# Optimization experiments

Hardware: AMD Instinct MI355X
Metric: run time of the kernel (lower is better)

Reference implementation:

```python
import jax, jax.numpy as jnp
import numpy as np

H_DIM = 1152
N_HEADS = 12
HEAD_DIM = H_DIM // N_HEADS  # 96, divisible by 3
SCALE_ROT = 32 // 16  # character_pixel_size // patch_size


def setup_inputs() -> dict:
    key = jax.random.key(0)
    ks = jax.random.split(key, 9)
    std = 1.0 / np.sqrt(H_DIM)
    return {
        "hidden_states": jax.random.normal(ks[0], (8, 1025, H_DIM), dtype=jnp.float32),
        "Wq": jax.random.normal(ks[1], (H_DIM, H_DIM), dtype=jnp.float32) * std,
        "bq": jax.random.normal(ks[2], (H_DIM,), dtype=jnp.float32) * 0.02,
        "Wk": jax.random.normal(ks[3], (H_DIM, H_DIM), dtype=jnp.float32) * std,
        "bk": jax.random.normal(ks[4], (H_DIM,), dtype=jnp.float32) * 0.02,
        "Wv": jax.random.normal(ks[5], (H_DIM, H_DIM), dtype=jnp.float32) * std,
        "bv": jax.random.normal(ks[6], (H_DIM,), dtype=jnp.float32) * 0.02,
        "Wo": jax.random.normal(ks[7], (H_DIM, H_DIM), dtype=jnp.float32) * std,
        "bo": jax.random.normal(ks[8], (H_DIM,), dtype=jnp.float32) * 0.02,
        "rows": 32,
        "cols": 32,
    }


def _rotary_tables(seq_len, rows, cols, dtype):
    # (seq_len, n_triplets) trig tables based on 2-D patch grid position
    inv_freq = 1.0 / (10000.0 ** (jnp.arange(0, HEAD_DIM, 3, dtype=dtype) / (HEAD_DIM * SCALE_ROT)))
    ids = jnp.arange(seq_len)
    cls_offset = 1 if seq_len != rows * cols else 0
    grid_ids = jnp.clip(ids - cls_offset, 0)
    row_ids = (grid_ids // cols).astype(dtype)
    col_ids = (grid_ids % cols).astype(dtype)
    theta = row_ids[:, None] * inv_freq
    psi = col_ids[:, None] * inv_freq
    return jnp.cos(theta), jnp.sin(theta), jnp.cos(psi), jnp.sin(psi)


def _apply_rotary_3d(x, ct, st, cp, sp):
    # x: (b, s, h, d) -> view as (b, s, h, t, 3)
    b, s, h, d = x.shape
    x = x.reshape(b, s, h, d // 3, 3)
    ct = ct[None, :, None, :]
    st = st[None, :, None, :]
    cp = cp[None, :, None, :]
    sp = sp[None, :, None, :]
    x0, x1, x2 = x[..., 0], x[..., 1], x[..., 2]
    r0 = cp * x0 + sp * st * x1 + sp * ct * x2
    r1 = ct * x1 - st * x2
    r2 = -sp * x0 + cp * st * x1 + cp * ct * x2
    return jnp.stack((r0, r1, r2), axis=-1).reshape(b, s, h, d)


def reference(hidden_states, Wq, bq, Wk, bk, Wv, bv, Wo, bo, rows, cols):
    b, s, _ = hidden_states.shape
    dtype = hidden_states.dtype
    scale = HEAD_DIM ** -0.5

    q = (hidden_states @ Wq + bq).reshape(b, s, N_HEADS, HEAD_DIM)
    k = (hidden_states @ Wk + bk).reshape(b, s, N_HEADS, HEAD_DIM)
    v = (hidden_states @ Wv + bv).reshape(b, s, N_HEADS, HEAD_DIM)

    ct, st, cp, sp = _rotary_tables(s, rows, cols, dtype)
    q = _apply_rotary_3d(q, ct, st, cp, sp)
    k = _apply_rotary_3d(k, ct, st, cp, sp)

    # (b, h, s, s) attention scores
    scores = jnp.einsum("bqhd,bkhd->bhqk", q, k) * scale
    probs = jax.nn.softmax(scores.astype(jnp.float32), axis=-1).astype(dtype)
    ctx = jnp.einsum("bhqk,bkhd->bqhd", probs, v).reshape(b, s, H_DIM)
    out = ctx @ Wo + bo
    return out
```

## Files before the change

### kernel.cpp

```cpp
#include <hip/hip_runtime.h>
#include <stdint.h>

#define BATCH 8
#define SEQ   1025
#define HDIM  1152
#define NH    12
#define DH    96
#define MROWS (BATCH*SEQ)
#define N_QKV (3*HDIM)
#define KD    HDIM
#define NT2   18

typedef __attribute__((ext_vector_type(8))) short short8;
typedef __attribute__((ext_vector_type(4))) short short4_;
typedef __attribute__((ext_vector_type(4))) float float4_;
typedef __attribute__((ext_vector_type(16))) float f32x16;

#define AS1 __attribute__((address_space(1)))
#define AS3 __attribute__((address_space(3)))
#define BARM() do { asm volatile("" ::: "memory"); __builtin_amdgcn_s_barrier(); asm volatile("" ::: "memory"); } while (0)
#define LGKM0() do { asm volatile("s_waitcnt lgkmcnt(0)" ::: "memory"); __builtin_amdgcn_sched_barrier(0); } while (0)

__device__ inline float bf2f(short s) {
  union { unsigned u; float f; } x; x.u = ((unsigned)(unsigned short)s) << 16; return x.f;
}
__device__ inline short f2bf(float f) {
  union { float f; unsigned u; } x; x.f = f;
  unsigned r = (x.u + 0x7fffu + ((x.u >> 16) & 1u)) >> 16;
  return (short)r;
}

__global__ __launch_bounds__(256) void convx(const float* __restrict__ hs, short* __restrict__ X) {
  int i = blockIdx.x * 256 + threadIdx.x;
  float4_ v = ((const float4_*)hs)[i];
  short4_ o;
  o[0] = f2bf(v[0]); o[1] = f2bf(v[1]); o[2] = f2bf(v[2]); o[3] = f2bf(v[3]);
  ((short4_*)X)[i] = o;
}

__global__ __launch_bounds__(256) void convw_t(const float* __restrict__ W0,
                                               const float* __restrict__ W1,
                                               const float* __restrict__ W2,
                                               short* __restrict__ Wt) {
  __shared__ float T[64][65];
  const int z = blockIdx.z;
  const float* W = z == 0 ? W0 : (z == 1 ? W1 : W2);
  const int n0 = blockIdx.x * 64, k0 = blockIdx.y * 64;
  const int tid = threadIdx.x;
  const int r = tid >> 2, cq = (tid & 3) * 16;
#pragma unroll
  for (int u = 0; u < 4; ++u) {
    float4_ v = *(const float4_*)&W[(long)(k0 + r) * HDIM + n0 + cq + u * 4];
    T[r][cq + u * 4 + 0] = v[0]; T[r][cq + u * 4 + 1] = v[1];
    T[r][cq + u * 4 + 2] = v[2]; T[r][cq + u * 4 + 3] = v[3];
  }
  __syncthreads();
  const int n = tid >> 2, kq = (tid & 3) * 16;
  short out[16];
#pragma unroll
  for (int u = 0; u < 16; ++u) out[u] = f2bf(T[kq + u][n]);
  short* dst = Wt + (long)(z * HDIM + n0 + n) * KD + k0 + kq;
  *(short8*)dst = *(short8*)&out[0];
  *(short8*)(dst + 8) = *(short8*)&out[8];
}

template<int OUTF32>
__global__ __launch_bounds__(512, 2) void gemm256(
    const short* __restrict__ A, const short* __restrict__ Bt,
    const float* __restrict__ b0, const float* __restrict__ b1, const float* __restrict__ b2,
    void* __restrict__ Cout, const int N, const int MT) {
  __shared__ alignas(16) short Lds[65536];
  const int tid = threadIdx.x;
  const int l = tid & 63, w = tid >> 6;
  const int lrow = l & 15, lg = l >> 4;
  const int wr = w >> 2, wc = w & 3;

  const int nwg = gridDim.x;
  const int qq = nwg >> 3, r8 = nwg & 7;
  const int xcd = blockIdx.x & 7, loc = blockIdx.x >> 3;
  const int wg = (xcd < r8 ? xcd * (qq + 1) : r8 * (qq + 1) + (xcd - r8) * qq) + loc;
  const int mt = wg % MT, nt = wg / MT;
  const int m0 = mt * 256, n0 = nt * 256;

  const short* asrc[2]; const short* bsrc[2];
#pragma unroll
  for (int i = 0; i < 2; ++i) {
    int p = i * 512 + tid;
    int wl = (p & 7) ^ ((p >> 3) & 7);
    int row = ((p >> 3) << 1) | (wl >> 2);
    int kc = (wl & 3) * 8;
    int ra = m0 + row; if (ra > MROWS - 1) ra = MROWS - 1;
    int rb = n0 + row; if (rb > N - 1) rb = N - 1;
    asrc[i] = A + (long)ra * KD + kc;
    bsrc[i] = Bt + (long)rb * KD + kc;
  }

#define STAGEA(sb, kh, kt_, i) \
  __builtin_amdgcn_global_load_lds((const AS1 void*)(asrc[i] + (kt_) * 64 + (kh) * 32), \
      (AS3 void*)(&Lds[(sb) * 16384 + (kh) * 8192 + (i * 512 + tid) * 8]), 16, 0, 0)
#define STAGEB(sb, kh, kt_, i) \
  __builtin_amdgcn_global_load_lds((const AS1 void*)(bsrc[i] + (kt_) * 64 + (kh) * 32), \
      (AS3 void*)(&Lds[32768 + (sb) * 16384 + (kh) * 8192 + (i * 512 + tid) * 8]), 16, 0, 0)
#define LDA(dst, base, mi) { const int row_ = wr * 128 + (mi) * 16 + lrow; \
  dst = *(const short8*)&Lds[(base) + ((row_ >> 1) << 6) + \
      (((((row_ & 1) << 2) + lg) ^ ((row_ >> 1) & 7)) << 3)]; }
#define LDB(dst, base, nj) { const int row_ = wc * 64 + (nj) * 16 + lrow; \
  dst = *(const short8*)&Lds[(base) + ((row_ >> 1) << 6) + \
      (((((row_ & 1) << 2) + lg) ^ ((row_ >> 1) & 7)) << 3)]; }
#define MFMA16(a, b, c) __builtin_amdgcn_mfma_f32_16x16x32_bf16(a, b, c, 0, 0, 0)
#define MF16(mb, A0, A1, A2, A3) \
  acc[(mb)+0][0] = MFMA16(A0, bf0, acc[(mb)+0][0]); \
  acc[(mb)+0][1] = MFMA16(A0, bf1, acc[(mb)+0][1]); \
  acc[(mb)+0][2] = MFMA16(A0, bf2, acc[(mb)+0][2]); \
  acc[(mb)+0][3] = MFMA16(A0, bf3, acc[(mb)+0][3]); \
  acc[(mb)+1][0] = MFMA16(A1, bf0, acc[(mb)+1][0]); \
  acc[(mb)+1][1] = MFMA16(A1, bf1, acc[(mb)+1][1]); \
  acc[(mb)+1][2] = MFMA16(A1, bf2, acc[(mb)+1][2]); \
  acc[(mb)+1][3] = MFMA16(A1, bf3, acc[(mb)+1][3]); \
  acc[(mb)+2][0] = MFMA16(A2, bf0, acc[(mb)+2][0]); \
  acc[(mb)+2][1] = MFMA16(A2, bf1, acc[(mb)+2][1]); \
  acc[(mb)+2][2] = MFMA16(A2, bf2, acc[(mb)+2][2]); \
  acc[(mb)+2][3] = MFMA16(A2, bf3, acc[(mb)+2][3]); \
  acc[(mb)+3][0] = MFMA16(A3, bf0, acc[(mb)+3][0]); \
  acc[(mb)+3][1] = MFMA16(A3, bf1, acc[(mb)+3][1]); \
  acc[(mb)+3][2] = MFMA16(A3, bf2, acc[(mb)+3][2]); \
  acc[(mb)+3][3] = MFMA16(A3, bf3, acc[(mb)+3][3]);

  float4_ acc[8][4];
#pragma unroll
  for (int mi = 0; mi < 8; ++mi)
#pragma unroll
    for (int nj = 0; nj < 4; ++nj) acc[mi][nj] = (float4_)(0.f);

  STAGEA(0, 0, 0, 0); STAGEA(0, 0, 0, 1);
  STAGEB(0, 0, 0, 0); STAGEB(0, 0, 0, 1);
  STAGEA(0, 1, 0, 0); STAGEA(0, 1, 0, 1);
  STAGEB(0, 1, 0, 0); STAGEB(0, 1, 0, 1);
  asm volatile("s_waitcnt vmcnt(4)" ::: "memory");
  BARM();

  for (int kt = 0; kt < NT2; ++kt) {
    const int cb = kt & 1, sb = (kt + 1) & 1;
    const bool dost = (kt + 1) < NT2;
    const int aK0 = cb * 16384, aK1 = aK0 + 8192;
    const int bK0 = 32768 + cb * 16384, bK1 = bK0 + 8192;
    short8 af0, af1, af2, af3, bf0, bf1, bf2, bf3;

    LDB(bf0, bK0, 0); LDB(bf1, bK0, 1); LDB(bf2, bK0, 2); LDB(bf3, bK0, 3);
    LDA(af0, aK0, 0); LDA(af1, aK0, 1); LDA(af2, aK0, 2); LDA(af3, aK0, 3);
    if (dost) { STAGEA(sb, 0, kt + 1, 0); STAGEA(sb, 0, kt + 1, 1); }
    BARM();
    LGKM0();
    __builtin_amdgcn_s_setprio(1);
    MF16(0, af0, af1, af2, af3);
    __builtin_amdgcn_s_setprio(0);
    BARM();
    LDA(af0, aK0, 4); LDA(af1, aK0, 5); LDA(af2, aK0, 6); LDA(af3, aK0, 7);
    if (dost) { STAGEB(sb, 0, kt + 1, 0); STAGEB(sb, 0, kt + 1, 1); }
    BARM();
    LGKM0();
    __builtin_amdgcn_s_setprio(1);
    MF16(4, af0, af1, af2, af3);
    __builtin_amdgcn_s_setprio(0);
    if (dost) asm volatile("s_waitcnt vmcnt(4)" ::: "memory");
    else      asm volatile("s_waitcnt vmcnt(0)" ::: "memory");
    BARM();
    LDB(bf0, bK1, 0); LDB(bf1, bK1, 1); LDB(bf2, bK1, 2); LDB(bf3, bK1, 3);
    LDA(af0, aK1, 0); LDA(af1, aK1, 1); LDA(af2, aK1, 2); LDA(af3, aK1, 3);
    if (dost) { STAGEA(sb, 1, kt + 1, 0); STAGEA(sb, 1, kt + 1, 1); }
    BARM();
    LGKM0();
    __builtin_amdgcn_s_setprio(1);
    MF16(0, af0, af1, af2, af3);
    __builtin_amdgcn_s_setprio(0);
    BARM();
    LDA(af0, aK1, 4); LDA(af1, aK1, 5); LDA(af2, aK1, 6); LDA(af3, aK1, 7);
    if (dost) { STAGEB(sb, 1, kt + 1, 0); STAGEB(sb, 1, kt + 1, 1); }
    BARM();
    LGKM0();
    __builtin_amdgcn_s_setprio(1);
    MF16(4, af0, af1, af2, af3);
    __builtin_amdgcn_s_setprio(0);
    if (dost) asm volatile("s_waitcnt vmcnt(4)" ::: "memory");
    BARM();
  }

  float bias[4];
#pragma unroll
  for (int nj = 0; nj < 4; ++nj) {
    int cn = n0 + wc * 64 + nj * 16 + lrow;
    float bv_ = 0.f;
    if (cn < N) bv_ = (N == HDIM) ? b0[cn]
                                  : (cn < HDIM ? b0[cn] : (cn < 2 * HDIM ? b1[cn - HDIM] : b2[cn - 2 * HDIM]));
    bias[nj] = bv_;
  }
#pragma unroll
  for (int mi = 0; mi < 8; ++mi)
#pragma unroll
    for (int r = 0; r < 4; ++r) {
      int m = m0 + wr * 128 + mi * 16 + lg * 4 + r;
      if (m >= MROWS) continue;
#pragma unroll
      for (int nj = 0; nj < 4; ++nj) {
        int cn = n0 + wc * 64 + nj * 16 + lrow;
        if (cn >= N) continue;
        float v = acc[mi][nj][r] + bias[nj];
        if (OUTF32) ((float*)Cout)[(long)m * N + cn] = v;
        else        ((short*)Cout)[(long)m * N + cn] = f2bf(v);
      }
    }
#undef STAGEA
#undef STAGEB
#undef LDA
#undef LDB
#undef MFMA16
#undef MF16
}

__global__ __launch_bounds__(256) void rotary_q(short* __restrict__ QKV,
                                                const int* __restrict__ rowsp,
                                                const int* __restrict__ colsp) {
  int idx = blockIdx.x * 256 + threadIdx.x;
  if (idx >= MROWS * NH * 4) return;
  const int qt = idx & 3;
  const int hm = idx >> 2;
  const int h = hm % NH, m = hm / NH;
  const int s = m % SEQ;
  const int cols = colsp[0], rws = rowsp[0];
  const int off = (SEQ != rws * cols) ? 1 : 0;
  int gid = s - off; if (gid < 0) gid = 0;
  const float frow = (float)(gid / cols), fcol = (float)(gid % cols);
  union { short sh[24]; short8 v[3]; } u;
  short* p = QKV + (long)m * N_QKV + h * DH + qt * 24;
  u.v[0] = *(short8*)p; u.v[1] = *(short8*)(p + 8); u.v[2] = *(short8*)(p + 16);
#pragma unroll
  for (int t = 0; t < 8; ++t) {
    int j = qt * 8 + t;
    float invf = exp2f((float)(3 * j) * (-13.287712379549449f / 192.0f));
    float st, ct, sp, cp;
    __sincosf(frow * invf, &st, &ct);
    __sincosf(fcol * invf, &sp, &cp);
    float x0 = bf2f(u.sh[3 * t]), x1 = bf2f(u.sh[3 * t + 1]), x2 = bf2f(u.sh[3 * t + 2]);
    u.sh[3 * t]     = f2bf( cp * x0 + sp * st * x1 + sp * ct * x2);
    u.sh[3 * t + 1] = f2bf( ct * x1 - st * x2);
    u.sh[3 * t + 2] = f2bf(-sp * x0 + cp * st * x1 + cp * ct * x2);
  }
  *(short8*)p = u.v[0]; *(short8*)(p + 8) = u.v[1]; *(short8*)(p + 16) = u.v[2];
}

__global__ __launch_bounds__(256) void fragpack(const short* __restrict__ QKV,
                                                short* __restrict__ Kf,
                                                short* __restrict__ Vf,
                                                const int* __restrict__ rowsp,
                                                const int* __restrict__ colsp) {
  __shared__ short L[64 * 96];
  const int t = blockIdx.x, bh = blockIdx.y;
  const int b = bh / NH, h = bh % NH;
  const int tid = threadIdx.x;
#pragma unroll
  for (int i = 0; i < 3; ++i) {
    int cc = i * 256 + tid;
    int kv = cc / 384;
    int rm = cc % 384;
    int r = rm / 12, m = rm % 12;
    int s = t * 32 + r; if (s > SEQ - 1) s = SEQ - 1;
    const short* src = QKV + (long)(b * SEQ + s) * N_QKV + (kv ? 2 * HDIM : HDIM) + h * DH + m * 8;
    *(short8*)&L[cc * 8] = *(const short8*)src;
  }
  __syncthreads();
  {
    const int cols = colsp[0], rws = rowsp[0];
    const int off = (SEQ != rws * cols) ? 1 : 0;
#pragma unroll
    for (int i = 0; i < 4; ++i) {
      int idx2 = i * 256 + tid;
      int r = idx2 >> 5, j = idx2 & 31;
      int s = t * 32 + r; if (s > SEQ - 1) s = SEQ - 1;
      int gid = s - off; if (gid < 0) gid = 0;
      float invf = exp2f((float)(3 * j) * (-13.287712379549449f / 192.0f));
      float st, ct, sp, cp;
      __sincosf((float)(gid / cols) * invf, &st, &ct);
      __sincosf((float)(gid % cols) * invf, &sp, &cp);
      short* pp = &L[r * 96 + 3 * j];
      float x0 = bf2f(pp[0]), x1 = bf2f(pp[1]), x2 = bf2f(pp[2]);
      pp[0] = f2bf( cp * x0 + sp * st * x1 + sp * ct * x2);
      pp[1] = f2bf( ct * x1 - st * x2);
      pp[2] = f2bf(-sp * x0 + cp * st * x1 + cp * ct * x2);
    }
  }
  __syncthreads();
#pragma unroll
  for (int i = 0; i < 3; ++i) {
    int oc = i * 256 + tid;
    if (oc < 384) {
      int c = oc / 64, ll = oc & 63;
      int qi = ll & 31, hi = ll >> 5;
      short8 v = *(const short8*)&L[qi * 96 + c * 16 + hi * 8];
      *(short8*)(Kf + (((long)(bh * 33 + t) * 6 + c) * 64 + ll) * 8) = v;
    } else {
      int oc2 = oc - 384;
      int d = oc2 / 128, sl = (oc2 / 64) & 1, ll = oc2 & 63;
      int qi = ll & 31, hi = ll >> 5;
      short8 v;
#pragma unroll
      for (int j = 0; j < 8; ++j)
        v[j] = L[32 * 96 + (sl * 16 + hi * 8 + j) * 96 + d * 32 + qi];
      *(short8*)(Vf + ((((long)(bh * 33 + t) * 3 + d) * 2 + sl) * 64 + ll) * 8) = v;
    }
  }
}

__global__ __launch_bounds__(128, 3) void attn_kernel(const short* __restrict__ QKV,
                                                      const short* __restrict__ Kf,
                                                      const short* __restrict__ Vf,
                                                      short* __restrict__ CTX) {
  const int tid = threadIdx.x;
  const int l = tid & 63, w = tid >> 6;
  const int qi = l & 31, hi = l >> 5;
  const int bid = blockIdx.x;
  const int xcd = bid & 7, jj = bid >> 3;
  const int bh = xcd * 12 + jj / 17;
  const int qb = jj % 17;
  const int b = bh / NH, h = bh % NH;
  const int s = qb * 64 + w * 32 + qi;
  const int sq = s > SEQ - 1 ? SEQ - 1 : s;

  const float scale = 0.1020620726159658f;
  const short* Qr = QKV + (long)(b * SEQ + sq) * N_QKV + h * DH;
  short8 qf[6];
#pragma unroll
  for (int c = 0; c < 6; ++c) {
    short8 v = *(const short8*)(Qr + c * 16 + hi * 8);
#pragma unroll
    for (int j = 0; j < 8; ++j) v[j] = f2bf(bf2f(v[j]) * scale);
    qf[c] = v;
  }

  const short* Kb = Kf + (long)bh * 33 * 6 * 64 * 8;
  const short* Vb = Vf + (long)bh * 33 * 6 * 64 * 8;

  f32x16 ctxv[3];
#pragma unroll
  for (int d = 0; d < 3; ++d) ctxv[d] = (f32x16)(0.f);
  float m_ = -1e30f, l_ = 0.f;

  for (int t = 0; t < 33; ++t) {
    f32x16 S = (f32x16)(0.f);
#pragma unroll
    for (int c = 0; c < 6; ++c) {
      short8 kf = *(const short8*)(Kb + (((long)t * 6 + c) * 64 + l) * 8);
      S = __builtin_amdgcn_mfma_f32_32x32x16_bf16(kf, qf[c], S, 0, 0, 0);
    }
    if (t == 32) {
      S[0] = hi ? -1e30f : S[0];
#pragma unroll
      for (int r = 1; r < 16; ++r) S[r] = -1e30f;
    }
    float tm = S[0];
#pragma unroll
    for (int r = 1; r < 16; ++r) tm = fmaxf(tm, S[r]);
    tm = fmaxf(tm, __shfl_xor(tm, 32));
    if (!__all(tm - m_ <= 8.f)) {
      float mn = fmaxf(m_, tm);
      float alpha = __expf(m_ - mn);
      m_ = mn;
      l_ *= alpha;
#pragma unroll
      for (int d = 0; d < 3; ++d)
#pragma unroll
        for (int r = 0; r < 16; ++r) ctxv[d][r] *= alpha;
    }
    float ts = 0.f;
#pragma unroll
    for (int r = 0; r < 16; ++r) { float p = __expf(S[r] - m_); S[r] = p; ts += p; }
    ts += __shfl_xor(ts, 32);
    l_ += ts;

    unsigned pk_[8];
#pragma unroll
    for (int j = 0; j < 8; ++j)
      pk_[j] = (unsigned)(unsigned short)f2bf(S[2 * j]) |
               ((unsigned)(unsigned short)f2bf(S[2 * j + 1]) << 16);
    unsigned s0 = hi ? pk_[0] : pk_[2];
    unsigned s1 = hi ? pk_[1] : pk_[3];
    unsigned s2 = hi ? pk_[4] : pk_[6];
    unsigned s3 = hi ? pk_[5] : pk_[7];
    unsigned r0 = __shfl_xor(s0, 32);
    unsigned r1 = __shfl_xor(s1, 32);
    unsigned r2 = __shfl_xor(s2, 32);
    unsigned r3 = __shfl_xor(s3, 32);
    union PF { unsigned u[4]; short8 s8; } f0, f1;
    f0.u[0] = hi ? r0 : pk_[0];
    f0.u[1] = hi ? r1 : pk_[1];
    f0.u[2] = hi ? pk_[2] : r0;
    f0.u[3] = hi ? pk_[3] : r1;
    f1.u[0] = hi ? r2 : pk_[4];
    f1.u[1] = hi ? r3 : pk_[5];
    f1.u[2] = hi ? pk_[6] : r2;
    f1.u[3] = hi ? pk_[7] : r3;

#pragma unroll
    for (int d = 0; d < 3; ++d) {
      const short* Vr = Vb + (((long)t * 3 + d) * 2 * 64) * 8;
      short8 vf0 = *(const short8*)(Vr + l * 8);
      ctxv[d] = __builtin_amdgcn_mfma_f32_32x32x16_bf16(vf0, f0.s8, ctxv[d], 0, 0, 0);
      short8 vf1 = *(const short8*)(Vr + (64 + l) * 8);
      ctxv[d] = __builtin_amdgcn_mfma_f32_32x32x16_bf16(vf1, f1.s8, ctxv[d], 0, 0, 0);
    }
  }

  float invl = 1.f / l_;
  if (s <= SEQ - 1) {
    short* Cr = CTX + (long)(b * SEQ + s) * HDIM + h * DH;
#pragma unroll
    for (int d = 0; d < 3; ++d)
#pragma unroll
      for (int g = 0; g < 4; ++g) {
        short4_ o;
#pragma unroll
        for (int r = 0; r < 4; ++r) o[r] = f2bf(ctxv[d][4 * g + r] * invl);
        *(short4_*)(Cr + d * 32 + 8 * g + 4 * hi) = o;
      }
  }
}

extern "C" void kernel_launch(void* const* d_in, const int* in_sizes, int n_in,
                              void* d_out, int out_size, void* d_ws, size_t ws_size,
                              hipStream_t stream) {
  const float* hs = (const float*)d_in[0];
  const float* Wq = (const float*)d_in[1];
  const float* bq = (const float*)d_in[2];
  const float* Wk = (const float*)d_in[3];
  const float* bk = (const float*)d_in[4];
  const float* Wv = (const float*)d_in[5];
  const float* bv = (const float*)d_in[6];
  const float* Wo = (const float*)d_in[7];
  const float* bo = (const float*)d_in[8];
  const int* rows = (const int*)d_in[9];
  const int* cols = (const int*)d_in[10];
  float* out = (float*)d_out;

  char* ws = (char*)d_ws;
  short* X   = (short*)(ws);
  short* Wt  = (short*)(ws + 18892800);
  short* Wot = (short*)(ws + 26855424);
  short* QKV = (short*)(ws + 29509632);
  short* Vf  = (short*)(ws + 86188032);
  short* CTX = (short*)(ws + 105652224);
  short* Kf  = (short*)(ws);

  convx<<<9225, 256, 0, stream>>>(hs, X);
  convw_t<<<dim3(18, 18, 3), 256, 0, stream>>>(Wq, Wk, Wv, Wt);
  convw_t<<<dim3(18, 18, 1), 256, 0, stream>>>(Wo, Wo, Wo, Wot);
  gemm256<0><<<462, 512, 0, stream>>>(X, Wt, bq, bk, bv, QKV, N_QKV, 33);
  rotary_q<<<1538, 256, 0, stream>>>(QKV, rows, cols);
  fragpack<<<dim3(33, 96), 256, 0, stream>>>(QKV, Kf, Vf, rows, cols);
  attn_kernel<<<1632, 128, 0, stream>>>(QKV, Kf, Vf, CTX);
  gemm256<1><<<165, 512, 0, stream>>>(CTX, Wot, bo, bo, bo, out, HDIM, 33);
}
```

Before: 275.3 us.

## Ping-pong wave groups in GEMM so LDS reads overlap MFMA of other half

Splits the 8 waves of the 256x256 GEMM into two groups by row half that alternate phases: one group reads its full A/B fragments from LDS while the other runs 32 MFMAs. Global-to-LDS staging for the next k-tile is issued as whole k-halves per phase, with adjusted vmcnt waits. The aim is to keep the matrix units busy while LDS reads are in flight. In exchange each thread holds 8 A fragments at once, raising register pressure under launch_bounds(512,2). It also relies on subtle barrier and waitcnt ordering for the shared double buffer.

After: 320.0 us. +16.2%, slower.

```diff
diff --git a/kernel.cpp b/kernel.cpp
--- a/kernel.cpp
+++ b/kernel.cpp
@@ -74,6 +74,7 @@
   const int l = tid & 63, w = tid >> 6;
   const int lrow = l & 15, lg = l >> 4;
   const int wr = w >> 2, wc = w & 3;
+  const bool isA = (wr == 0);
 
   const int nwg = gridDim.x;
   const int qq = nwg >> 3, r8 = nwg & 7;
@@ -101,12 +102,19 @@
 #define STAGEB(sb, kh, kt_, i) \
   __builtin_amdgcn_global_load_lds((const AS1 void*)(bsrc[i] + (kt_) * 64 + (kh) * 32), \
       (AS3 void*)(&Lds[32768 + (sb) * 16384 + (kh) * 8192 + (i * 512 + tid) * 8]), 16, 0, 0)
+#define STAGE_KH(sb, kh, kt_) do { \
+  STAGEA(sb, kh, kt_, 0); STAGEA(sb, kh, kt_, 1); \
+  STAGEB(sb, kh, kt_, 0); STAGEB(sb, kh, kt_, 1); } while (0)
 #define LDA(dst, base, mi) { const int row_ = wr * 128 + (mi) * 16 + lrow; \
   dst = *(const short8*)&Lds[(base) + ((row_ >> 1) << 6) + \
       (((((row_ & 1) << 2) + lg) ^ ((row_ >> 1) & 7)) << 3)]; }
 #define LDB(dst, base, nj) { const int row_ = wc * 64 + (nj) * 16 + lrow; \
   dst = *(const short8*)&Lds[(base) + ((row_ >> 1) << 6) + \
       (((((row_ & 1) << 2) + lg) ^ ((row_ >> 1) & 7)) << 3)]; }
+#define RD(aB, bB) do { \
+  LDB(bf0, bB, 0); LDB(bf1, bB, 1); LDB(bf2, bB, 2); LDB(bf3, bB, 3); \
+  LDA(af0, aB, 0); LDA(af1, aB, 1); LDA(af2, aB, 2); LDA(af3, aB, 3); \
+  LDA(af4, aB, 4); LDA(af5, aB, 5); LDA(af6, aB, 6); LDA(af7, aB, 7); } while (0)
 #define MFMA16(a, b, c) __builtin_amdgcn_mfma_f32_16x16x32_bf16(a, b, c, 0, 0, 0)
 #define MF16(mb, A0, A1, A2, A3) \
   acc[(mb)+0][0] = MFMA16(A0, bf0, acc[(mb)+0][0]); \
@@ -125,65 +133,49 @@
   acc[(mb)+3][1] = MFMA16(A3, bf1, acc[(mb)+3][1]); \
   acc[(mb)+3][2] = MFMA16(A3, bf2, acc[(mb)+3][2]); \
   acc[(mb)+3][3] = MFMA16(A3, bf3, acc[(mb)+3][3]);
+#define MF32() do { \
+  __builtin_amdgcn_s_setprio(1); \
+  MF16(0, af0, af1, af2, af3); \
+  MF16(4, af4, af5, af6, af7); \
+  __builtin_amdgcn_s_setprio(0); } while (0)
 
   float4_ acc[8][4];
 #pragma unroll
   for (int mi = 0; mi < 8; ++mi)
 #pragma unroll
     for (int nj = 0; nj < 4; ++nj) acc[mi][nj] = (float4_)(0.f);
-
-  STAGEA(0, 0, 0, 0); STAGEA(0, 0, 0, 1);
-  STAGEB(0, 0, 0, 0); STAGEB(0, 0, 0, 1);
-  STAGEA(0, 1, 0, 0); STAGEA(0, 1, 0, 1);
-  STAGEB(0, 1, 0, 0); STAGEB(0, 1, 0, 1);
+  short8 af0, af1, af2, af3, af4, af5, af6, af7, bf0, bf1, bf2, bf3;
+
+  STAGE_KH(0, 0, 0);
+  STAGE_KH(0, 1, 0);
   asm volatile("s_waitcnt vmcnt(4)" ::: "memory");
   BARM();
 
   for (int kt = 0; kt < NT2; ++kt) {
-    const int cb = kt & 1, sb = (kt + 1) & 1;
+    const int cb = kt & 1, sbuf = cb ^ 1;
     const bool dost = (kt + 1) < NT2;
     const int aK0 = cb * 16384, aK1 = aK0 + 8192;
     const int bK0 = 32768 + cb * 16384, bK1 = bK0 + 8192;
-    short8 af0, af1, af2, af3, bf0, bf1, bf2, bf3;
-
-    LDB(bf0, bK0, 0); LDB(bf1, bK0, 1); LDB(bf2, bK0, 2); LDB(bf3, bK0, 3);
-    LDA(af0, aK0, 0); LDA(af1, aK0, 1); LDA(af2, aK0, 2); LDA(af3, aK0, 3);
-    if (dost) { STAGEA(sb, 0, kt + 1, 0); STAGEA(sb, 0, kt + 1, 1); }
+
+    if (dost) STAGE_KH(sbuf, 0, kt + 1);
+    if (isA) { RD(aK0, bK0); }
+    else if (kt > 0) { LGKM0(); MF32(); }
     BARM();
-    LGKM0();
-    __builtin_amdgcn_s_setprio(1);
-    MF16(0, af0, af1, af2, af3);
-    __builtin_amdgcn_s_setprio(0);
-    BARM();
-    LDA(af0, aK0, 4); LDA(af1, aK0, 5); LDA(af2, aK0, 6); LDA(af3, aK0, 7);
-    if (dost) { STAGEB(sb, 0, kt + 1, 0); STAGEB(sb, 0, kt + 1, 1); }
-    BARM();
-    LGKM0();
-    __builtin_amdgcn_s_setprio(1);
-    MF16(4, af0, af1, af2, af3);
-    __builtin_amdgcn_s_setprio(0);
-    if (dost) asm volatile("s_waitcnt vmcnt(4)" ::: "memory");
+    if (dost) STAGE_KH(sbuf, 1, kt + 1);
+    if (isA) { LGKM0(); MF32(); }
+    else { RD(aK0, bK0); }
+    if (dost) asm volatile("s_waitcnt vmcnt(8)" ::: "memory");
     else      asm volatile("s_waitcnt vmcnt(0)" ::: "memory");
     BARM();
-    LDB(bf0, bK1, 0); LDB(bf1, bK1, 1); LDB(bf2, bK1, 2); LDB(bf3, bK1, 3);
-    LDA(af0, aK1, 0); LDA(af1, aK1, 1); LDA(af2, aK1, 2); LDA(af3, aK1, 3);
-    if (dost) { STAGEA(sb, 1, kt + 1, 0); STAGEA(sb, 1, kt + 1, 1); }
+    if (isA) { RD(aK1, bK1); }
+    else { LGKM0(); MF32(); }
     BARM();
-    LGKM0();
-    __builtin_amdgcn_s_setprio(1);
-    MF16(0, af0, af1, af2, af3);
-    __builtin_amdgcn_s_setprio(0);
-    BARM();
-    LDA(af0, aK1, 4); LDA(af1, aK1, 5); LDA(af2, aK1, 6); LDA(af3, aK1, 7);
-    if (dost) { STAGEB(sb, 1, kt + 1, 0); STAGEB(sb, 1, kt + 1, 1); }
-    BARM();
-    LGKM0();
-    __builtin_amdgcn_s_setprio(1);
-    MF16(4, af0, af1, af2, af3);
-    __builtin_amdgcn_s_setprio(0);
+    if (isA) { LGKM0(); MF32(); }
+    else { RD(aK1, bK1); }
     if (dost) asm volatile("s_waitcnt vmcnt(4)" ::: "memory");
     BARM();
   }
+  if (!isA) { LGKM0(); MF32(); }
 
   float bias[4];
 #pragma unroll
@@ -211,10 +203,13 @@
     }
 #undef STAGEA
 #undef STAGEB
+#undef STAGE_KH
 #undef LDA
 #undef LDB
+#undef RD
 #undef MFMA16
 #undef MF16
+#undef MF32
 }
 
 __global__ __launch_bounds__(256) void rotary_q(short* __restrict__ QKV,
```

## Merge rotary and fragpack launches; use 128-tile GEMM for output projection

Applied to the files above, without the earlier changes.

Combines the Q rotary kernel and the K/V rotary fragment-pack kernel into one launch. Block ranges pick which role a block plays, which removes one launch and lets the two independent pieces of work overlap. Replaces the 256-tile output-projection GEMM (165 blocks) with a new 128x128-tile GEMM using a 3-stage LDS pipeline (585 blocks), so more of the GPU's compute units are busy. The smaller tiles bring more redundant global loads and lower per-block arithmetic intensity.

Result: faster. 267.0 us (-3.0%).

```diff
diff --git a/kernel.cpp b/kernel.cpp
--- a/kernel.cpp
+++ b/kernel.cpp
@@ -10,6 +10,7 @@
 #define N_QKV (3*HDIM)
 #define KD    HDIM
 #define NT2   18
+#define NTK   36
 
 typedef __attribute__((ext_vector_type(8))) short short8;
 typedef __attribute__((ext_vector_type(4))) short short4_;
@@ -217,60 +218,147 @@
 #undef MF16
 }
 
-__global__ __launch_bounds__(256) void rotary_q(short* __restrict__ QKV,
-                                                const int* __restrict__ rowsp,
-                                                const int* __restrict__ colsp) {
-  int idx = blockIdx.x * 256 + threadIdx.x;
-  if (idx >= MROWS * NH * 4) return;
-  const int qt = idx & 3;
-  const int hm = idx >> 2;
-  const int h = hm % NH, m = hm / NH;
-  const int s = m % SEQ;
+template<int OUTF32>
+__global__ __launch_bounds__(256, 3) void gemm128(
+    const short* __restrict__ A, const short* __restrict__ Bt,
+    const float* __restrict__ b0,
+    void* __restrict__ Cout, const int N, const int MT) {
+  __shared__ alignas(16) short Lds[24576];
+  const int tid = threadIdx.x;
+  const int l = tid & 63, w = tid >> 6;
+  const int lrow = l & 15, lg = l >> 4;
+  const int wr = w >> 1, wc = w & 1;
+
+  const int nwg = gridDim.x;
+  const int qq = nwg >> 3, r8 = nwg & 7;
+  const int xcd = blockIdx.x & 7, loc = blockIdx.x >> 3;
+  const int wg = (xcd < r8 ? xcd * (qq + 1) : r8 * (qq + 1) + (xcd - r8) * qq) + loc;
+  const int mt = wg % MT, nt = wg / MT;
+  const int m0 = mt * 128, n0 = nt * 128;
+
+  const short* asrc[2]; const short* bsrc[2];
+#pragma unroll
+  for (int i = 0; i < 2; ++i) {
+    int p = i * 256 + tid;
+    int wl = (p & 7) ^ ((p >> 3) & 7);
+    int row = ((p >> 3) << 1) | (wl >> 2);
+    int kc = (wl & 3) * 8;
+    int ra = m0 + row; if (ra > MROWS - 1) ra = MROWS - 1;
+    int rb = n0 + row; if (rb > N - 1) rb = N - 1;
+    asrc[i] = A + (long)ra * KD + kc;
+    bsrc[i] = Bt + (long)rb * KD + kc;
+  }
+
+#define STAGEA(bi, kt_, i) \
+  __builtin_amdgcn_global_load_lds((const AS1 void*)(asrc[i] + (kt_) * 32), \
+      (AS3 void*)(&Lds[(bi) * 4096 + (i * 256 + tid) * 8]), 16, 0, 0)
+#define STAGEB(bi, kt_, i) \
+  __builtin_amdgcn_global_load_lds((const AS1 void*)(bsrc[i] + (kt_) * 32), \
+      (AS3 void*)(&Lds[12288 + (bi) * 4096 + (i * 256 + tid) * 8]), 16, 0, 0)
+#define LDA(dst, abase, mi) { const int row_ = wr * 64 + (mi) * 16 + lrow; \
+  dst = *(const short8*)&Lds[(abase) + ((row_ >> 1) << 6) + \
+      (((((row_ & 1) << 2) + lg) ^ ((row_ >> 1) & 7)) << 3)]; }
+#define LDB(dst, bbase, nj) { const int row_ = wc * 64 + (nj) * 16 + lrow; \
+  dst = *(const short8*)&Lds[(bbase) + ((row_ >> 1) << 6) + \
+      (((((row_ & 1) << 2) + lg) ^ ((row_ >> 1) & 7)) << 3)]; }
+#define MFMA16(a, b, c) __builtin_amdgcn_mfma_f32_16x16x32_bf16(a, b, c, 0, 0, 0)
+
+  float4_ acc[4][4];
+#pragma unroll
+  for (int mi = 0; mi < 4; ++mi)
+#pragma unroll
+    for (int nj = 0; nj < 4; ++nj) acc[mi][nj] = (float4_)(0.f);
+
+  STAGEA(0, 0, 0); STAGEA(0, 0, 1); STAGEB(0, 0, 0); STAGEB(0, 0, 1);
+  STAGEA(1, 1, 0); STAGEA(1, 1, 1); STAGEB(1, 1, 0); STAGEB(1, 1, 1);
+  asm volatile("s_waitcnt vmcnt(4)" ::: "memory");
+  BARM();
+
+  for (int kt = 0; kt < NTK; ++kt) {
+    const int cur = kt % 3, st = (kt + 2) % 3;
+    const bool dost = (kt + 2) < NTK;
+    const int abase = cur * 4096, bbase = 12288 + cur * 4096;
+    if (dost) {
+      STAGEA(st, kt + 2, 0); STAGEA(st, kt + 2, 1);
+      STAGEB(st, kt + 2, 0); STAGEB(st, kt + 2, 1);
+    }
+    short8 a0, a1, a2, a3, bb0, bb1, bb2, bb3;
+    LDB(bb0, bbase, 0); LDB(bb1, bbase, 1); LDB(bb2, bbase, 2); LDB(bb3, bbase, 3);
+    LDA(a0, abase, 0); LDA(a1, abase, 1); LDA(a2, abase, 2); LDA(a3, abase, 3);
+    acc[0][0] = MFMA16(a0, bb0, acc[0][0]);
+    acc[0][1] = MFMA16(a0, bb1, acc[0][1]);
+    acc[0][2] = MFMA16(a0, bb2, acc[0][2]);
+    acc[0][3] = MFMA16(a0, bb3, acc[0][3]);
+    acc[1][0] = MFMA16(a1, bb0, acc[1][0]);
+    acc[1][1] = MFMA16(a1, bb1, acc[1][1]);
+    acc[1][2] = MFMA16(a1, bb2, acc[1][2]);
+    acc[1][3] = MFMA16(a1, bb3, acc[1][3]);
+    acc[2][0] = MFMA16(a2, bb0, acc[2][0]);
+    acc[2][1] = MFMA16(a2, bb1, acc[2][1]);
+    acc[2][2] = MFMA16(a2, bb2, acc[2][2]);
+    acc[2][3] = MFMA16(a2, bb3, acc[2][3]);
+    acc[3][0] = MFMA16(a3, bb0, acc[3][0]);
+    acc[3][1] = MFMA16(a3, bb1, acc[3][1]);
+    acc[3][2] = MFMA16(a3, bb2, acc[3][2]);
+    acc[3][3] = MFMA16(a3, bb3, acc[3][3]);
+    if (dost)                asm volatile("s_waitcnt vmcnt(4)" ::: "memory");
+    else if (kt == NTK - 2)  asm volatile("s_waitcnt vmcnt(0)" ::: "memory");
+    asm volatile("s_waitcnt lgkmcnt(0)" ::: "memory");
+    BARM();
+  }
+
+  float bias[4];
+#pragma unroll
+  for (int nj = 0; nj < 4; ++nj) {
+    int cn = n0 + wc * 64 + nj * 16 + lrow;
+    bias[nj] = (cn < N) ? b0[cn] : 0.f;
+  }
+#pragma unroll
+  for (int mi = 0; mi < 4; ++mi)
+#pragma unroll
+    for (int r = 0; r < 4; ++r) {
+      int m = m0 + wr * 64 + mi * 16 + lg * 4 + r;
+      if (m >= MROWS) continue;
+#pragma unroll
+      for (int nj = 0; nj < 4; ++nj) {
+        int cn = n0 + wc * 64 + nj * 16 + lrow;
+        if (cn >= N) continue;
+        float v = acc[mi][nj][r] + bias[nj];
+        if (OUTF32) ((float*)Cout)[(long)m * N + cn] = v;
+        else        ((short*)Cout)[(long)m * N + cn] = f2bf(v);
+      }
+    }
+#undef STAGEA
+#undef STAGEB
+#undef LDA
+#undef LDB
+#undef MFMA16
+}
+
+__global__ __launch_bounds__(256) void rotpack(short* __restrict__ QKV,
+                                               short* __restrict__ Kf,
+                                               short* __restrict__ Vf,
+                                               const int* __restrict__ rowsp,
+                                               const int* __restrict__ colsp) {
+  __shared__ short L[64 * 96];
+  const int tid = threadIdx.x;
   const int cols = colsp[0], rws = rowsp[0];
   const int off = (SEQ != rws * cols) ? 1 : 0;
-  int gid = s - off; if (gid < 0) gid = 0;
-  const float frow = (float)(gid / cols), fcol = (float)(gid % cols);
-  union { short sh[24]; short8 v[3]; } u;
-  short* p = QKV + (long)m * N_QKV + h * DH + qt * 24;
-  u.v[0] = *(short8*)p; u.v[1] = *(short8*)(p + 8); u.v[2] = *(short8*)(p + 16);
-#pragma unroll
-  for (int t = 0; t < 8; ++t) {
-    int j = qt * 8 + t;
-    float invf = exp2f((float)(3 * j) * (-13.287712379549449f / 192.0f));
-    float st, ct, sp, cp;
-    __sincosf(frow * invf, &st, &ct);
-    __sincosf(fcol * invf, &sp, &cp);
-    float x0 = bf2f(u.sh[3 * t]), x1 = bf2f(u.sh[3 * t + 1]), x2 = bf2f(u.sh[3 * t + 2]);
-    u.sh[3 * t]     = f2bf( cp * x0 + sp * st * x1 + sp * ct * x2);
-    u.sh[3 * t + 1] = f2bf( ct * x1 - st * x2);
-    u.sh[3 * t + 2] = f2bf(-sp * x0 + cp * st * x1 + cp * ct * x2);
-  }
-  *(short8*)p = u.v[0]; *(short8*)(p + 8) = u.v[1]; *(short8*)(p + 16) = u.v[2];
-}
-
-__global__ __launch_bounds__(256) void fragpack(const short* __restrict__ QKV,
-                                                short* __restrict__ Kf,
-                                                short* __restrict__ Vf,
-                                                const int* __restrict__ rowsp,
-                                                const int* __restrict__ colsp) {
-  __shared__ short L[64 * 96];
-  const int t = blockIdx.x, bh = blockIdx.y;
-  const int b = bh / NH, h = bh % NH;
-  const int tid = threadIdx.x;
-#pragma unroll
-  for (int i = 0; i < 3; ++i) {
-    int cc = i * 256 + tid;
-    int kv = cc / 384;
-    int rm = cc % 384;
-    int r = rm / 12, m = rm % 12;
-    int s = t * 32 + r; if (s > SEQ - 1) s = SEQ - 1;
-    const short* src = QKV + (long)(b * SEQ + s) * N_QKV + (kv ? 2 * HDIM : HDIM) + h * DH + m * 8;
-    *(short8*)&L[cc * 8] = *(const short8*)src;
-  }
-  __syncthreads();
-  {
-    const int cols = colsp[0], rws = rowsp[0];
-    const int off = (SEQ != rws * cols) ? 1 : 0;
+
+  if (blockIdx.x < 3168) {
+    const int t = blockIdx.x % 33, bh = blockIdx.x / 33;
+    const int b = bh / NH, h = bh % NH;
+#pragma unroll
+    for (int i = 0; i < 3; ++i) {
+      int cc = i * 256 + tid;
+      int kv = cc / 384;
+      int rm = cc % 384;
+      int r = rm / 12, m = rm % 12;
+      int s = t * 32 + r; if (s > SEQ - 1) s = SEQ - 1;
+      const short* src = QKV + (long)(b * SEQ + s) * N_QKV + (kv ? 2 * HDIM : HDIM) + h * DH + m * 8;
+      *(short8*)&L[cc * 8] = *(const short8*)src;
+    }
+    __syncthreads();
 #pragma unroll
     for (int i = 0; i < 4; ++i) {
       int idx2 = i * 256 + tid;
@@ -287,26 +375,51 @@
       pp[1] = f2bf( ct * x1 - st * x2);
       pp[2] = f2bf(-sp * x0 + cp * st * x1 + cp * ct * x2);
     }
-  }
-  __syncthreads();
-#pragma unroll
-  for (int i = 0; i < 3; ++i) {
-    int oc = i * 256 + tid;
-    if (oc < 384) {
-      int c = oc / 64, ll = oc & 63;
-      int qi = ll & 31, hi = ll >> 5;
-      short8 v = *(const short8*)&L[qi * 96 + c * 16 + hi * 8];
-      *(short8*)(Kf + (((long)(bh * 33 + t) * 6 + c) * 64 + ll) * 8) = v;
-    } else {
-      int oc2 = oc - 384;
-      int d = oc2 / 128, sl = (oc2 / 64) & 1, ll = oc2 & 63;
-      int qi = ll & 31, hi = ll >> 5;
-      short8 v;
-#pragma unroll
-      for (int j = 0; j < 8; ++j)
-        v[j] = L[32 * 96 + (sl * 16 + hi * 8 + j) * 96 + d * 32 + qi];
-      *(short8*)(Vf + ((((long)(bh * 33 + t) * 3 + d) * 2 + sl) * 64 + ll) * 8) = v;
-    }
+    __syncthreads();
+#pragma unroll
+    for (int i = 0; i < 3; ++i) {
+      int oc = i * 256 + tid;
+      if (oc < 384) {
+        int c = oc / 64, ll = oc & 63;
+        int qi = ll & 31, hi = ll >> 5;
+        short8 v = *(const short8*)&L[qi * 96 + c * 16 + hi * 8];
+        *(short8*)(Kf + (((long)(bh * 33 + t) * 6 + c) * 64 + ll) * 8) = v;
+      } else {
+        int oc2 = oc - 384;
+        int d = oc2 / 128, sl = (oc2 / 64) & 1, ll = oc2 & 63;
+        int qi = ll & 31, hi = ll >> 5;
+        short8 v;
+#pragma unroll
+        for (int j = 0; j < 8; ++j)
+          v[j] = L[32 * 96 + (sl * 16 + hi * 8 + j) * 96 + d * 32 + qi];
+        *(short8*)(Vf + ((((long)(bh * 33 + t) * 3 + d) * 2 + sl) * 64 + ll) * 8) = v;
+      }
+    }
+  } else {
+    int idx = (blockIdx.x - 3168) * 256 + tid;
+    if (idx >= MROWS * NH * 4) return;
+    const int qt = idx & 3;
+    const int hm = idx >> 2;
+    const int h = hm % NH, m = hm / NH;
+    const int s = m % SEQ;
+    int gid = s - off; if (gid < 0) gid = 0;
+    const float frow = (float)(gid / cols), fcol = (float)(gid % cols);
+    union { short sh[24]; short8 v[3]; } u;
+    short* p = QKV + (long)m * N_QKV + h * DH + qt * 24;
+    u.v[0] = *(short8*)p; u.v[1] = *(short8*)(p + 8); u.v[2] = *(short8*)(p + 16);
+#pragma unroll
+    for (int t = 0; t < 8; ++t) {
+      int j = qt * 8 + t;
+      float invf = exp2f((float)(3 * j) * (-13.287712379549449f / 192.0f));
+      float st, ct, sp, cp;
+      __sincosf(frow * invf, &st, &ct);
+      __sincosf(fcol * invf, &sp, &cp);
+      float x0 = bf2f(u.sh[3 * t]), x1 = bf2f(u.sh[3 * t + 1]), x2 = bf2f(u.sh[3 * t + 2]);
+      u.sh[3 * t]     = f2bf( cp * x0 + sp * st * x1 + sp * ct * x2);
+      u.sh[3 * t + 1] = f2bf( ct * x1 - st * x2);
+      u.sh[3 * t + 2] = f2bf(-sp * x0 + cp * st * x1 + cp * ct * x2);
+    }
+    *(short8*)p = u.v[0]; *(short8*)(p + 8) = u.v[1]; *(short8*)(p + 16) = u.v[2];
   }
 }
 
@@ -453,8 +566,7 @@
   convw_t<<<dim3(18, 18, 3), 256, 0, stream>>>(Wq, Wk, Wv, Wt);
   convw_t<<<dim3(18, 18, 1), 256, 0, stream>>>(Wo, Wo, Wo, Wot);
   gemm256<0><<<462, 512, 0, stream>>>(X, Wt, bq, bk, bv, QKV, N_QKV, 33);
-  rotary_q<<<1538, 256, 0, stream>>>(QKV, rows, cols);
-  fragpack<<<dim3(33, 96), 256, 0, stream>>>(QKV, Kf, Vf, rows, cols);
+  rotpack<<<3168 + 1538, 256, 0, stream>>>(QKV, Kf, Vf, rows, cols);
   attn_kernel<<<1632, 128, 0, stream>>>(QKV, Kf, Vf, CTX);
-  gemm256<1><<<165, 512, 0, stream>>>(CTX, Wot, bo, bo, bo, out, HDIM, 33);
-}
+  gemm128<1><<<585, 256, 0, stream>>>(CTX, Wot, bo, out, HDIM, 65);
+}
```
